# Kernel optimization log

Hardware: AMD Instinct MI355X
Metric: run time of the kernel (lower is better)

## Reference

```python
import jax, jax.numpy as jnp
import numpy as np


def setup_inputs() -> dict:
    key = jax.random.key(0)
    k0, k1, k2, k3 = jax.random.split(key, 4)
    N, D, DEG, B = 20000, 128, 32, 1024
    features = jax.random.normal(k0, (N, D), jnp.float32)
    neighbors = jax.random.randint(k1, (N, DEG), 0, N, dtype=jnp.int32)
    train_index = jax.random.randint(k2, (B,), 0, N, dtype=jnp.int32)
    W = jax.random.normal(k3, (1, 2 * D), jnp.float32) * (1.0 / np.sqrt(2 * D))
    b = jnp.zeros((1,), jnp.float32)
    return {"features": features, "W": W, "b": b, "neighbors": neighbors,
            "train_index": train_index, "walk_times": 8, "batch_size": B}


def reference(features, W, b, neighbors, train_index, walk_times, batch_size):
    N, D = features.shape
    B = train_index.shape[0]
    rows = jnp.arange(B)[:, None]                       # [B,1]
    self_oh = jax.nn.one_hot(train_index, N, dtype=jnp.float32)  # [B,N]

    # Dense adjacency rows of the start nodes (== adj_sparse[batch] densified)
    nb0 = neighbors[train_index]                        # [B,deg]
    adj0 = jnp.zeros((B, N), jnp.float32).at[rows, nb0].set(1.0)

    chosen = self_oh                                    # visited mask (start node marked)
    candi_mask = (adj0 - chosen) > 0.0                  # non-self candidates

    # Per-edge learned score: relu(Linear(concat(f_x, f_y))) == relu(fx@Wx + fy@Wy + b)
    Wx, Wy = W[0, :D], W[0, D:]
    sx = features[train_index] @ Wx                     # [B]
    sy = features[nb0] @ Wy                             # [B,deg]
    s = jax.nn.relu(sx[:, None] + sy + b[0])            # [B,deg]
    scored = jnp.zeros((B, N), jnp.float32).at[rows, nb0].set(s)
    candi = jnp.where(candi_mask, scored, 0.0)
    # rows with no (or all-zero-scored) candidates fall back to a self-loop of weight 1
    candi = jnp.where((candi.sum(axis=1) == 0.0)[:, None], self_oh, candi)

    keys = jax.random.split(jax.random.key(42), walk_times)

    def step(carry, k):
        candi, chosen = carry
        # degenerate rows: resample the start node (safe fallback for empty support)
        p = jnp.where((candi.sum(axis=1) == 0.0)[:, None], self_oh, candi)
        # multinomial(p, 1) via Gumbel-max (categorical with probs proportional to p)
        logp = jnp.where(p > 0.0, jnp.log(jnp.where(p > 0.0, p, 1.0)), -jnp.inf)
        g = jax.random.gumbel(k, (p.shape[0], p.shape[1]), jnp.float32)
        new = jnp.argmax(logp + g, axis=1)              # [B]
        chosen = jnp.maximum(chosen, jax.nn.one_hot(new, p.shape[1], dtype=jnp.float32))
        adj_new = jnp.zeros_like(candi).at[rows, neighbors[new]].set(1.0)
        candi = ((candi - chosen + adj_new) > 0.0).astype(jnp.float32)
        return (candi, chosen), new

    (_, _), steps = jax.lax.scan(step, (candi, chosen), keys)  # steps: [T,B]
    walks = jnp.concatenate(
        [train_index[:, None].astype(jnp.int32), steps.T.astype(jnp.int32)], axis=1)
    return walks
```

## Files before the change

kernel.cpp:

```cpp
#include <hip/hip_runtime.h>
#include <cstdint>

namespace {

constexpr int N    = 20000;
constexpr int D    = 128;
constexpr int DEG  = 32;
constexpr int BB   = 1024;
constexpr int T    = 8;
constexpr int NC   = (N + 15) / 16;
constexpr int MAXC = 384;

__device__ __forceinline__ uint32_t rotl32(uint32_t x, int n) {
  return (x << n) | (x >> (32 - n));
}

__device__ __forceinline__ void threefry2x32(uint32_t k0, uint32_t k1,
                                             uint32_t x0, uint32_t x1,
                                             uint32_t& o0, uint32_t& o1) {
  const uint32_t ks2 = k0 ^ k1 ^ 0x1BD11BDAu;
  x0 += k0; x1 += k1;
#define TF_ROUND(r) { x0 += x1; x1 = rotl32(x1, (r)); x1 ^= x0; }
  TF_ROUND(13) TF_ROUND(15) TF_ROUND(26) TF_ROUND(6)
  x0 += k1;  x1 += ks2 + 1u;
  TF_ROUND(17) TF_ROUND(29) TF_ROUND(16) TF_ROUND(24)
  x0 += ks2; x1 += k0 + 2u;
  TF_ROUND(13) TF_ROUND(15) TF_ROUND(26) TF_ROUND(6)
  x0 += k0;  x1 += k1 + 3u;
  TF_ROUND(17) TF_ROUND(29) TF_ROUND(16) TF_ROUND(24)
  x0 += k1;  x1 += ks2 + 4u;
  TF_ROUND(13) TF_ROUND(15) TF_ROUND(26) TF_ROUND(6)
  x0 += ks2; x1 += k0 + 5u;
#undef TF_ROUND
  o0 = x0; o1 = x1;
}

__device__ __forceinline__ uint32_t rbits(uint32_t k0, uint32_t k1, uint32_t j) {
  uint32_t o0, o1;
  threefry2x32(k0, k1, 0u, j, o0, o1);
  return o0 ^ o1;
}

__device__ __forceinline__ float gumbel_f32(uint32_t bits) {
  const uint32_t mant = bits >> 9;
  const float u = (mant == 0u) ? 1.17549435e-38f
                               : (__uint_as_float(0x3F800000u | mant) - 1.0f);
  const float inner = -(float)log((double)u);
  return -(float)log((double)inner);
}

__device__ __forceinline__ uint32_t f2ord(float f) {
  const uint32_t b = __float_as_uint(f);
  return (b & 0x80000000u) ? ~b : (b | 0x80000000u);
}

template <int CTRL>
__device__ __forceinline__ uint32_t dppmov(uint32_t v) {
  return (uint32_t)__builtin_amdgcn_update_dpp((int)v, (int)v, CTRL, 0xF, 0xF, false);
}

__device__ __forceinline__ void wave_max64(uint32_t& hi, uint32_t& lo) {
#define RL(CTRL) { const uint32_t oh = dppmov<CTRL>(hi), ol = dppmov<CTRL>(lo); \
    if (oh > hi || (oh == hi && ol > lo)) { hi = oh; lo = ol; } }
  RL(0x111) RL(0x112) RL(0x114) RL(0x118) RL(0x142) RL(0x143)
#undef RL
  hi = (uint32_t)__builtin_amdgcn_readlane((int)hi, 63);
  lo = (uint32_t)__builtin_amdgcn_readlane((int)lo, 63);
}

__device__ __forceinline__ uint32_t cwd(int n)  { return (uint32_t)n >> 4; }
__device__ __forceinline__ uint32_t cbit(int n) { return 1u << (((uint32_t)n & 15u) << 1); }

__global__ __launch_bounds__(64)
void walk_kernel(const float* __restrict__ features,
                 const float* __restrict__ W,
                 const float* __restrict__ bptr,
                 const int*   __restrict__ neighbors,
                 const int*   __restrict__ train_index,
                 int* __restrict__ out)
{
  __shared__ uint32_t comb[NC];
  __shared__ int      lst[MAXC];
  __shared__ float    val0[DEG];

  const int lane = threadIdx.x;
  const int r    = blockIdx.x;
  const int self = train_index[r];
  const uint32_t rN = (uint32_t)(r * N);
  const uint64_t lower = (1ULL << lane) - 1ULL;

  int nbj = -1;
  if (lane < DEG) nbj = neighbors[(size_t)self * DEG + lane];

  {
    uint64_t* c8 = reinterpret_cast<uint64_t*>(comb);
    for (int i = lane; i < NC / 2; i += 64) c8[i] = 0ull;
  }

  uint32_t sk0, sk1;
  threefry2x32(0u, 42u, 0u, (uint32_t)lane, sk0, sk1);

  const float bval = bptr[0];
  const float* frow = features + (size_t)self * D;
  float acc = frow[lane] * W[lane] + frow[lane + 64] * W[lane + 64];
  for (int m = 1; m < 64; m <<= 1) acc += __shfl_xor(acc, m);
  const float sx = acc;

  float sval = 0.0f;
  if (lane < DEG) {
    const float* g  = features + (size_t)nbj * D;
    const float* wy = W + D;
    float a = 0.0f;
    for (int d = 0; d < D; d += 4) {
      const float4 f = *reinterpret_cast<const float4*>(g + d);
      const float4 w = *reinterpret_cast<const float4*>(wy + d);
      a += f.x * w.x; a += f.y * w.y; a += f.z * w.z; a += f.w * w.w;
    }
    sval = fmaxf((sx + a) + bval, 0.0f);
  }

  bool add0 = false;
  if (lane < DEG && nbj != self && sval > 0.0f) {
    const uint32_t old = atomicOr(&comb[cwd(nbj)], cbit(nbj));
    add0 = !(old & cbit(nbj));
  }
  const uint64_t m0 = __ballot(add0);
  if (add0) {
    const int p = (int)__popcll(m0 & lower);
    lst[p] = nbj; val0[p] = sval;
  }
  int cnt = (int)__popcll(m0);
  if (lane == 0) {
    atomicOr(&comb[cwd(self)], cbit(self) << 1);
    if (cnt == 0) {
      lst[0] = self; val0[0] = 1.0f;
      atomicOr(&comb[cwd(self)], cbit(self));
    }
  }
  if (cnt == 0) cnt = 1;

  int zom0 = 0, zom1 = 0, zom2 = 0, zom3 = 0, zmask = 0;
  uint32_t hiP = 0u, loP = 0u;

  for (int k = 0; k < T; ++k) {
    uint32_t hi, lo;
    if (k == 0) {
      const uint32_t kk0 = (uint32_t)__builtin_amdgcn_readlane((int)sk0, 0);
      const uint32_t kk1 = (uint32_t)__builtin_amdgcn_readlane((int)sk1, 0);
      hi = 0u; lo = 0u;
      if (lane < cnt) {
        const int c = lst[lane];
        const float v = (float)log((double)val0[lane])
                      + gumbel_f32(rbits(kk0, kk1, rN + (uint32_t)c));
        hi = f2ord(v); lo = ((0x7FFFFFu - (uint32_t)c) << 9) | (uint32_t)lane;
      }
    } else {
      hi = hiP; lo = loP;
    }
    wave_max64(hi, lo);
    const bool haveList = (cnt > 0);
    const int nn  = haveList ? (int)(0x7FFFFFu - (lo >> 9)) : self;
    const int pos = (int)(lo & 0x1FFu);

    if (lane == 0) out[r * (T + 1) + k + 1] = nn;
    if (k == T - 1) break;

    int nb = -1;
    if (lane < DEG) nb = neighbors[(size_t)nn * DEG + lane];

    if (lane == 0) atomicOr(&comb[cwd(nn)], cbit(nn) << 1);

    float v0f = 1.0f;
    if (k == 0 && haveList) v0f = val0[pos];

    if (haveList) {
      const int last = lst[cnt - 1];
      if (pos != cnt - 1 && lane == 0) lst[pos] = last;
      --cnt;
    }

    const uint32_t nk0 = (uint32_t)__builtin_amdgcn_readlane((int)sk0, k + 1);
    const uint32_t nk1 = (uint32_t)__builtin_amdgcn_readlane((int)sk1, k + 1);

    hiP = 0u; loP = 0u;
    for (int i = lane; i < cnt; i += 64) {
      const int c = lst[i];
      const uint32_t h = rbits(nk0, nk1, rN + (uint32_t)c) >> 9;
      const uint32_t l = ((0x7FFFFFu - (uint32_t)c) << 9) | (uint32_t)i;
      if (h > hiP || (h == hiP && l > loP)) { hiP = h; loP = l; }
    }

    const bool adNN = __any(nb == nn);
    const bool wasZ = ((zmask & 1) && zom0 == nn) || ((zmask & 2) && zom1 == nn) ||
                      ((zmask & 4) && zom2 == nn) || ((zmask & 8) && zom3 == nn);
    const bool stay = haveList &&
        ((k == 0) ? (((v0f - 1.0f) + (adNN ? 1.0f : 0.0f)) > 0.0f) : adNN);

    if (stay) {
      if (lane == 0) lst[cnt] = nn;
      const int posN = cnt; ++cnt;
      if (!wasZ) {
        if      (!(zmask & 1)) { zom0 = nn; zmask |= 1; }
        else if (!(zmask & 2)) { zom1 = nn; zmask |= 2; }
        else if (!(zmask & 4)) { zom2 = nn; zmask |= 4; }
        else                   { zom3 = nn; zmask |= 8; }
      }
      const uint32_t h = rbits(nk0, nk1, rN + (uint32_t)nn) >> 9;
      const uint32_t l = ((0x7FFFFFu - (uint32_t)nn) << 9) | (uint32_t)posN;
      if (h > hiP || (h == hiP && l > loP)) { hiP = h; loP = l; }
    } else if (wasZ) {
      if ((zmask & 1) && zom0 == nn) zmask &= ~1;
      else if ((zmask & 2) && zom1 == nn) zmask &= ~2;
      else if ((zmask & 4) && zom2 == nn) zmask &= ~4;
      else if ((zmask & 8) && zom3 == nn) zmask &= ~8;
    }

    bool zdrop = false;
    if (zmask) {
#define ZTEST(BIT, Z) \
      if ((zmask & BIT) && Z != nn) { \
        if (!__any(nb == Z)) { \
          int pz = -1; \
          for (int i = lane; i < cnt; i += 64) if (lst[i] == Z) pz = i; \
          const uint64_t fz = __ballot(pz >= 0); \
          const int sz = (int)(__ffsll((unsigned long long)fz) - 1); \
          pz = __shfl(pz, sz); \
          const int lastz = lst[cnt - 1]; \
          if (pz != cnt - 1 && lane == 0) lst[pz] = lastz; \
          --cnt; zmask &= ~BIT; zdrop = true; \
        } \
      }
      ZTEST(1, zom0) ZTEST(2, zom1) ZTEST(4, zom2) ZTEST(8, zom3)
#undef ZTEST
    }
    if (zdrop) {
      hiP = 0u; loP = 0u;
      for (int i = lane; i < cnt; i += 64) {
        const int c = lst[i];
        const uint32_t h = rbits(nk0, nk1, rN + (uint32_t)c) >> 9;
        const uint32_t l = ((0x7FFFFFu - (uint32_t)c) << 9) | (uint32_t)i;
        if (h > hiP || (h == hiP && l > loP)) { hiP = h; loP = l; }
      }
    }

    uint32_t hN = 0u;
    if (lane < DEG) hN = rbits(nk0, nk1, rN + (uint32_t)nb) >> 9;
    bool added = false;
    if (lane < DEG) {
      const uint32_t old = atomicOr(&comb[cwd(nb)], cbit(nb));
      added = !(old & (cbit(nb) | (cbit(nb) << 1)));
    }
    const uint64_t ma = __ballot(added);
    const int mypos = cnt + (int)__popcll(ma & lower);
    if (added) {
      lst[mypos] = nb;
      const uint32_t l = ((0x7FFFFFu - (uint32_t)nb) << 9) | (uint32_t)mypos;
      if (hN > hiP || (hN == hiP && l > loP)) { hiP = hN; loP = l; }
    }
    cnt += (int)__popcll(ma);
  }
  if (lane == 0) out[r * (T + 1)] = self;
}

}

extern "C" void kernel_launch(void* const* d_in, const int* in_sizes, int n_in,
                              void* d_out, int out_size, void* d_ws, size_t ws_size,
                              hipStream_t stream) {
  const float* features  = (const float*)d_in[0];
  const float* W         = (const float*)d_in[1];
  const float* b         = (const float*)d_in[2];
  const int*   neighbors = (const int*)d_in[3];
  const int*   tindex    = (const int*)d_in[4];
  int* out = (int*)d_out;

  hipLaunchKernelGGL(walk_kernel, dim3(BB), dim3(64), 0, stream,
                     features, W, b, neighbors, tindex, out);
}
```

Baseline: 24.12 us.

## Pack two walk rows per wavefront using 32-lane halves

Each 64-lane wavefront now handles two batch rows, one per 32-lane half, with separate shared visited bitmaps and candidate lists, and the grid is halved to BB/2 blocks. Before, lanes 32-63 sat idle during the neighbor-degree work. Reductions become half-wave DPP reductions that read lanes 31 and 63, and ballots are shifted per half. The cost is divergence when the two halves take different branches (zombie tests, list scans), which serializes their work, plus a doubled shared-memory footprint per block.

```diff
diff --git a/kernel.cpp b/kernel.cpp
--- a/kernel.cpp
+++ b/kernel.cpp
@@ -59,13 +59,16 @@
   return (uint32_t)__builtin_amdgcn_update_dpp((int)v, (int)v, CTRL, 0xF, 0xF, false);
 }
 
-__device__ __forceinline__ void wave_max64(uint32_t& hi, uint32_t& lo) {
+__device__ __forceinline__ void wave_max64_half(uint32_t& hi, uint32_t& lo, int half) {
 #define RL(CTRL) { const uint32_t oh = dppmov<CTRL>(hi), ol = dppmov<CTRL>(lo); \
     if (oh > hi || (oh == hi && ol > lo)) { hi = oh; lo = ol; } }
-  RL(0x111) RL(0x112) RL(0x114) RL(0x118) RL(0x142) RL(0x143)
+  RL(0x111) RL(0x112) RL(0x114) RL(0x118) RL(0x142)
 #undef RL
-  hi = (uint32_t)__builtin_amdgcn_readlane((int)hi, 63);
-  lo = (uint32_t)__builtin_amdgcn_readlane((int)lo, 63);
+  const uint32_t hA = (uint32_t)__builtin_amdgcn_readlane((int)hi, 31);
+  const uint32_t lA = (uint32_t)__builtin_amdgcn_readlane((int)lo, 31);
+  const uint32_t hB = (uint32_t)__builtin_amdgcn_readlane((int)hi, 63);
+  const uint32_t lB = (uint32_t)__builtin_amdgcn_readlane((int)lo, 63);
+  hi = half ? hB : hA; lo = half ? lB : lA;
 }
 
 __device__ __forceinline__ uint32_t cwd(int n)  { return (uint32_t)n >> 4; }
@@ -79,62 +82,68 @@
                  const int*   __restrict__ train_index,
                  int* __restrict__ out)
 {
-  __shared__ uint32_t comb[NC];
-  __shared__ int      lst[MAXC];
-  __shared__ float    val0[DEG];
+  __shared__ __align__(8) uint32_t comb[2][NC];
+  __shared__ int      lst[2][MAXC];
+  __shared__ float    val0[2][DEG];
 
   const int lane = threadIdx.x;
-  const int r    = blockIdx.x;
+  const int half = lane >> 5;
+  const int hl   = lane & 31;
+  const int bid  = blockIdx.x;
+  const int r    = bid + half * (BB / 2);
   const int self = train_index[r];
   const uint32_t rN = (uint32_t)(r * N);
-  const uint64_t lower = (1ULL << lane) - 1ULL;
-
-  int nbj = -1;
-  if (lane < DEG) nbj = neighbors[(size_t)self * DEG + lane];
+  const uint32_t lowerH = (1u << hl) - 1u;
+
+  const int nbj = neighbors[(size_t)self * DEG + hl];
 
   {
-    uint64_t* c8 = reinterpret_cast<uint64_t*>(comb);
-    for (int i = lane; i < NC / 2; i += 64) c8[i] = 0ull;
+    uint64_t* c8 = reinterpret_cast<uint64_t*>(&comb[0][0]);
+    for (int i = lane; i < NC; i += 64) c8[i] = 0ull;
   }
 
   uint32_t sk0, sk1;
   threefry2x32(0u, 42u, 0u, (uint32_t)lane, sk0, sk1);
 
   const float bval = bptr[0];
-  const float* frow = features + (size_t)self * D;
-  float acc = frow[lane] * W[lane] + frow[lane + 64] * W[lane + 64];
-  for (int m = 1; m < 64; m <<= 1) acc += __shfl_xor(acc, m);
-  const float sx = acc;
-
-  float sval = 0.0f;
-  if (lane < DEG) {
+  const int selfA = __shfl(self, 0);
+  const int selfB = __shfl(self, 32);
+  const float* frowA = features + (size_t)selfA * D;
+  float accA = frowA[lane] * W[lane] + frowA[lane + 64] * W[lane + 64];
+  for (int m = 1; m < 64; m <<= 1) accA += __shfl_xor(accA, m);
+  const float* frowB = features + (size_t)selfB * D;
+  float accB = frowB[lane] * W[lane] + frowB[lane + 64] * W[lane + 64];
+  for (int m = 1; m < 64; m <<= 1) accB += __shfl_xor(accB, m);
+  const float sx = half ? accB : accA;
+
+  float a = 0.0f;
+  {
     const float* g  = features + (size_t)nbj * D;
     const float* wy = W + D;
-    float a = 0.0f;
     for (int d = 0; d < D; d += 4) {
       const float4 f = *reinterpret_cast<const float4*>(g + d);
       const float4 w = *reinterpret_cast<const float4*>(wy + d);
       a += f.x * w.x; a += f.y * w.y; a += f.z * w.z; a += f.w * w.w;
     }
-    sval = fmaxf((sx + a) + bval, 0.0f);
-  }
-
-  bool add0 = false;
-  if (lane < DEG && nbj != self && sval > 0.0f) {
-    const uint32_t old = atomicOr(&comb[cwd(nbj)], cbit(nbj));
+  }
+  const float sval = fmaxf((sx + a) + bval, 0.0f);
+
+  bool add0 = (nbj != self && sval > 0.0f);
+  if (add0) {
+    const uint32_t old = atomicOr(&comb[half][cwd(nbj)], cbit(nbj));
     add0 = !(old & cbit(nbj));
   }
-  const uint64_t m0 = __ballot(add0);
+  const uint32_t m0 = (uint32_t)(__ballot(add0) >> (half << 5));
   if (add0) {
-    const int p = (int)__popcll(m0 & lower);
-    lst[p] = nbj; val0[p] = sval;
-  }
-  int cnt = (int)__popcll(m0);
-  if (lane == 0) {
-    atomicOr(&comb[cwd(self)], cbit(self) << 1);
+    const int p = (int)__popc(m0 & lowerH);
+    lst[half][p] = nbj; val0[half][p] = sval;
+  }
+  int cnt = (int)__popc(m0);
+  if (hl == 0) {
+    atomicOr(&comb[half][cwd(self)], cbit(self) << 1);
     if (cnt == 0) {
-      lst[0] = self; val0[0] = 1.0f;
-      atomicOr(&comb[cwd(self)], cbit(self));
+      lst[half][0] = self; val0[half][0] = 1.0f;
+      atomicOr(&comb[half][cwd(self)], cbit(self));
     }
   }
   if (cnt == 0) cnt = 1;
@@ -148,34 +157,34 @@
       const uint32_t kk0 = (uint32_t)__builtin_amdgcn_readlane((int)sk0, 0);
       const uint32_t kk1 = (uint32_t)__builtin_amdgcn_readlane((int)sk1, 0);
       hi = 0u; lo = 0u;
-      if (lane < cnt) {
-        const int c = lst[lane];
-        const float v = (float)log((double)val0[lane])
+      if (hl < cnt) {
+        const int c = lst[half][hl];
+        const float v = (float)log((double)val0[half][hl])
                       + gumbel_f32(rbits(kk0, kk1, rN + (uint32_t)c));
-        hi = f2ord(v); lo = ((0x7FFFFFu - (uint32_t)c) << 9) | (uint32_t)lane;
+        hi = f2ord(v); lo = ((0x7FFFFFu - (uint32_t)c) << 9) | (uint32_t)hl;
       }
     } else {
       hi = hiP; lo = loP;
     }
-    wave_max64(hi, lo);
+    wave_max64_half(hi, lo, half);
     const bool haveList = (cnt > 0);
     const int nn  = haveList ? (int)(0x7FFFFFu - (lo >> 9)) : self;
     const int pos = (int)(lo & 0x1FFu);
 
-    if (lane == 0) out[r * (T + 1) + k + 1] = nn;
+    if (hl == 0) out[r * (T + 1) + k + 1] = nn;
     if (k == T - 1) break;
 
-    int nb = -1;
-    if (lane < DEG) nb = neighbors[(size_t)nn * DEG + lane];
-
-    if (lane == 0) atomicOr(&comb[cwd(nn)], cbit(nn) << 1);
+    const int nb = neighbors[(size_t)nn * DEG + hl];
+
+    if (hl == 0) atomicOr(&comb[half][cwd(nn)], cbit(nn) << 1);
 
     float v0f = 1.0f;
-    if (k == 0 && haveList) v0f = val0[pos];
+    if (k == 0 && haveList) v0f = val0[half][pos];
+    int last = 0;
+    if (haveList) last = lst[half][cnt - 1];
 
     if (haveList) {
-      const int last = lst[cnt - 1];
-      if (pos != cnt - 1 && lane == 0) lst[pos] = last;
+      if (pos != cnt - 1 && hl == 0) lst[half][pos] = last;
       --cnt;
     }
 
@@ -183,21 +192,21 @@
     const uint32_t nk1 = (uint32_t)__builtin_amdgcn_readlane((int)sk1, k + 1);
 
     hiP = 0u; loP = 0u;
-    for (int i = lane; i < cnt; i += 64) {
-      const int c = lst[i];
+    for (int i = hl; i < cnt; i += 32) {
+      const int c = lst[half][i];
       const uint32_t h = rbits(nk0, nk1, rN + (uint32_t)c) >> 9;
       const uint32_t l = ((0x7FFFFFu - (uint32_t)c) << 9) | (uint32_t)i;
       if (h > hiP || (h == hiP && l > loP)) { hiP = h; loP = l; }
     }
 
-    const bool adNN = __any(nb == nn);
+    const bool adNN = ((uint32_t)(__ballot(nb == nn) >> (half << 5))) != 0u;
     const bool wasZ = ((zmask & 1) && zom0 == nn) || ((zmask & 2) && zom1 == nn) ||
                       ((zmask & 4) && zom2 == nn) || ((zmask & 8) && zom3 == nn);
     const bool stay = haveList &&
         ((k == 0) ? (((v0f - 1.0f) + (adNN ? 1.0f : 0.0f)) > 0.0f) : adNN);
 
     if (stay) {
-      if (lane == 0) lst[cnt] = nn;
+      if (hl == 0) lst[half][cnt] = nn;
       const int posN = cnt; ++cnt;
       if (!wasZ) {
         if      (!(zmask & 1)) { zom0 = nn; zmask |= 1; }
@@ -219,14 +228,14 @@
     if (zmask) {
 #define ZTEST(BIT, Z) \
       if ((zmask & BIT) && Z != nn) { \
-        if (!__any(nb == Z)) { \
+        if (((uint32_t)(__ballot(nb == Z) >> (half << 5))) == 0u) { \
           int pz = -1; \
-          for (int i = lane; i < cnt; i += 64) if (lst[i] == Z) pz = i; \
-          const uint64_t fz = __ballot(pz >= 0); \
-          const int sz = (int)(__ffsll((unsigned long long)fz) - 1); \
+          for (int i = hl; i < cnt; i += 32) if (lst[half][i] == Z) pz = i; \
+          const uint32_t fz = (uint32_t)(__ballot(pz >= 0) >> (half << 5)); \
+          const int sz = (half << 5) + (__ffs(fz) - 1); \
           pz = __shfl(pz, sz); \
-          const int lastz = lst[cnt - 1]; \
-          if (pz != cnt - 1 && lane == 0) lst[pz] = lastz; \
+          const int lastz = lst[half][cnt - 1]; \
+          if (pz != cnt - 1 && hl == 0) lst[half][pz] = lastz; \
           --cnt; zmask &= ~BIT; zdrop = true; \
         } \
       }
@@ -235,31 +244,27 @@
     }
     if (zdrop) {
       hiP = 0u; loP = 0u;
-      for (int i = lane; i < cnt; i += 64) {
-        const int c = lst[i];
+      for (int i = hl; i < cnt; i += 32) {
+        const int c = lst[half][i];
         const uint32_t h = rbits(nk0, nk1, rN + (uint32_t)c) >> 9;
         const uint32_t l = ((0x7FFFFFu - (uint32_t)c) << 9) | (uint32_t)i;
         if (h > hiP || (h == hiP && l > loP)) { hiP = h; loP = l; }
       }
     }
 
-    uint32_t hN = 0u;
-    if (lane < DEG) hN = rbits(nk0, nk1, rN + (uint32_t)nb) >> 9;
-    bool added = false;
-    if (lane < DEG) {
-      const uint32_t old = atomicOr(&comb[cwd(nb)], cbit(nb));
-      added = !(old & (cbit(nb) | (cbit(nb) << 1)));
-    }
-    const uint64_t ma = __ballot(added);
-    const int mypos = cnt + (int)__popcll(ma & lower);
+    const uint32_t hN = rbits(nk0, nk1, rN + (uint32_t)nb) >> 9;
+    const uint32_t old = atomicOr(&comb[half][cwd(nb)], cbit(nb));
+    const bool added = !(old & (cbit(nb) | (cbit(nb) << 1)));
+    const uint32_t ma = (uint32_t)(__ballot(added) >> (half << 5));
+    const int mypos = cnt + (int)__popc(ma & lowerH);
     if (added) {
-      lst[mypos] = nb;
+      lst[half][mypos] = nb;
       const uint32_t l = ((0x7FFFFFu - (uint32_t)nb) << 9) | (uint32_t)mypos;
       if (hN > hiP || (hN == hiP && l > loP)) { hiP = hN; loP = l; }
     }
-    cnt += (int)__popcll(ma);
-  }
-  if (lane == 0) out[r * (T + 1)] = self;
+    cnt += (int)__popc(ma);
+  }
+  if (hl == 0) out[r * (T + 1)] = self;
 }
 
 }
@@ -274,6 +279,6 @@
   const int*   tindex    = (const int*)d_in[4];
   int* out = (int*)d_out;
 
-  hipLaunchKernelGGL(walk_kernel, dim3(BB), dim3(64), 0, stream,
+  hipLaunchKernelGGL(walk_kernel, dim3(BB / 2), dim3(64), 0, stream,
                      features, W, b, neighbors, tindex, out);
 }
```

Result: slower. 26.32 us (+9.1%).

## Keep candidate list in per-lane registers instead of shared memory

Applied to the files above, without the earlier changes.

Moves the candidate node list from a shared-memory array into five per-lane register slots (c0..c4), and uses readlane for lookups and lane-predicated writes for swap-removal and insertion. Newly added neighbours are still written to a shared staging buffer and then copied into the register slots. The goal is to drop LDS reads from the per-step scoring loops and the removal searches. In exchange it adds branchy slot selection and more register use, and it caps capacity at 320 entries where the shared array held 384.

```diff
diff --git a/kernel.cpp b/kernel.cpp
--- a/kernel.cpp
+++ b/kernel.cpp
@@ -3,13 +3,14 @@
 
 namespace {
 
-constexpr int N    = 20000;
-constexpr int D    = 128;
-constexpr int DEG  = 32;
-constexpr int BB   = 1024;
-constexpr int T    = 8;
-constexpr int NC   = (N + 15) / 16;
-constexpr int MAXC = 384;
+constexpr int N     = 20000;
+constexpr int D     = 128;
+constexpr int DEG   = 32;
+constexpr int BB    = 1024;
+constexpr int T     = 8;
+constexpr int NC    = (N + 15) / 16;
+constexpr int MAXC  = 320;
+constexpr int SLOTS = 5;
 
 __device__ __forceinline__ uint32_t rotl32(uint32_t x, int n) {
   return (x << n) | (x >> (32 - n));
@@ -71,6 +72,8 @@
 __device__ __forceinline__ uint32_t cwd(int n)  { return (uint32_t)n >> 4; }
 __device__ __forceinline__ uint32_t cbit(int n) { return 1u << (((uint32_t)n & 15u) << 1); }
 
+#define GETC(S) ((S)==0?c0:(S)==1?c1:(S)==2?c2:(S)==3?c3:c4)
+
 __global__ __launch_bounds__(64)
 void walk_kernel(const float* __restrict__ features,
                  const float* __restrict__ W,
@@ -79,8 +82,8 @@
                  const int*   __restrict__ train_index,
                  int* __restrict__ out)
 {
-  __shared__ uint32_t comb[NC];
-  __shared__ int      lst[MAXC];
+  __shared__ __align__(8) uint32_t comb[NC];
+  __shared__ int      stage[MAXC];
   __shared__ float    val0[DEG];
 
   const int lane = threadIdx.x;
@@ -88,6 +91,8 @@
   const int self = train_index[r];
   const uint32_t rN = (uint32_t)(r * N);
   const uint64_t lower = (1ULL << lane) - 1ULL;
+
+  int c0 = 0, c1 = 0, c2 = 0, c3 = 0, c4 = 0;
 
   int nbj = -1;
   if (lane < DEG) nbj = neighbors[(size_t)self * DEG + lane];
@@ -127,17 +132,22 @@
   const uint64_t m0 = __ballot(add0);
   if (add0) {
     const int p = (int)__popcll(m0 & lower);
-    lst[p] = nbj; val0[p] = sval;
+    stage[p] = nbj; val0[p] = sval;
   }
   int cnt = (int)__popcll(m0);
   if (lane == 0) {
     atomicOr(&comb[cwd(self)], cbit(self) << 1);
     if (cnt == 0) {
-      lst[0] = self; val0[0] = 1.0f;
+      val0[0] = 1.0f;
       atomicOr(&comb[cwd(self)], cbit(self));
     }
   }
-  if (cnt == 0) cnt = 1;
+  if (cnt == 0) {
+    if (lane == 0) c0 = self;
+    cnt = 1;
+  } else if (lane < cnt) {
+    c0 = stage[lane];
+  }
 
   int zom0 = 0, zom1 = 0, zom2 = 0, zom3 = 0, zmask = 0;
   uint32_t hiP = 0u, loP = 0u;
@@ -149,7 +159,7 @@
       const uint32_t kk1 = (uint32_t)__builtin_amdgcn_readlane((int)sk1, 0);
       hi = 0u; lo = 0u;
       if (lane < cnt) {
-        const int c = lst[lane];
+        const int c = c0;
         const float v = (float)log((double)val0[lane])
                       + gumbel_f32(rbits(kk0, kk1, rN + (uint32_t)c));
         hi = f2ord(v); lo = ((0x7FFFFFu - (uint32_t)c) << 9) | (uint32_t)lane;
@@ -174,8 +184,23 @@
     if (k == 0 && haveList) v0f = val0[pos];
 
     if (haveList) {
-      const int last = lst[cnt - 1];
-      if (pos != cnt - 1 && lane == 0) lst[pos] = last;
+      const int li = cnt - 1;
+      int last;
+      { const int ls = li >> 6, ll = li & 63;
+        if      (ls == 0) last = __builtin_amdgcn_readlane(c0, ll);
+        else if (ls == 1) last = __builtin_amdgcn_readlane(c1, ll);
+        else if (ls == 2) last = __builtin_amdgcn_readlane(c2, ll);
+        else if (ls == 3) last = __builtin_amdgcn_readlane(c3, ll);
+        else              last = __builtin_amdgcn_readlane(c4, ll);
+      }
+      if (pos != li) {
+        const int ps = pos >> 6, pl = pos & 63;
+        if      (ps == 0) { if (lane == pl) c0 = last; }
+        else if (ps == 1) { if (lane == pl) c1 = last; }
+        else if (ps == 2) { if (lane == pl) c2 = last; }
+        else if (ps == 3) { if (lane == pl) c3 = last; }
+        else              { if (lane == pl) c4 = last; }
+      }
       --cnt;
     }
 
@@ -183,11 +208,15 @@
     const uint32_t nk1 = (uint32_t)__builtin_amdgcn_readlane((int)sk1, k + 1);
 
     hiP = 0u; loP = 0u;
-    for (int i = lane; i < cnt; i += 64) {
-      const int c = lst[i];
-      const uint32_t h = rbits(nk0, nk1, rN + (uint32_t)c) >> 9;
-      const uint32_t l = ((0x7FFFFFu - (uint32_t)c) << 9) | (uint32_t)i;
-      if (h > hiP || (h == hiP && l > loP)) { hiP = h; loP = l; }
+#pragma unroll
+    for (int s = 0; s < SLOTS; ++s) {
+      const int idx = s * 64 + lane;
+      if (idx < cnt) {
+        const int c = GETC(s);
+        const uint32_t h = rbits(nk0, nk1, rN + (uint32_t)c) >> 9;
+        const uint32_t l = ((0x7FFFFFu - (uint32_t)c) << 9) | (uint32_t)idx;
+        if (h > hiP || (h == hiP && l > loP)) { hiP = h; loP = l; }
+      }
     }
 
     const bool adNN = __any(nb == nn);
@@ -197,8 +226,15 @@
         ((k == 0) ? (((v0f - 1.0f) + (adNN ? 1.0f : 0.0f)) > 0.0f) : adNN);
 
     if (stay) {
-      if (lane == 0) lst[cnt] = nn;
-      const int posN = cnt; ++cnt;
+      const int posN = cnt;
+      { const int ps = posN >> 6, pl = posN & 63;
+        if      (ps == 0) { if (lane == pl) c0 = nn; }
+        else if (ps == 1) { if (lane == pl) c1 = nn; }
+        else if (ps == 2) { if (lane == pl) c2 = nn; }
+        else if (ps == 3) { if (lane == pl) c3 = nn; }
+        else              { if (lane == pl) c4 = nn; }
+      }
+      ++cnt;
       if (!wasZ) {
         if      (!(zmask & 1)) { zom0 = nn; zmask |= 1; }
         else if (!(zmask & 2)) { zom1 = nn; zmask |= 2; }
@@ -221,12 +257,31 @@
       if ((zmask & BIT) && Z != nn) { \
         if (!__any(nb == Z)) { \
           int pz = -1; \
-          for (int i = lane; i < cnt; i += 64) if (lst[i] == Z) pz = i; \
+          if (0 * 64 + lane < cnt && c0 == Z) pz = 0 * 64 + lane; \
+          if (1 * 64 + lane < cnt && c1 == Z) pz = 1 * 64 + lane; \
+          if (2 * 64 + lane < cnt && c2 == Z) pz = 2 * 64 + lane; \
+          if (3 * 64 + lane < cnt && c3 == Z) pz = 3 * 64 + lane; \
+          if (4 * 64 + lane < cnt && c4 == Z) pz = 4 * 64 + lane; \
           const uint64_t fz = __ballot(pz >= 0); \
           const int sz = (int)(__ffsll((unsigned long long)fz) - 1); \
           pz = __shfl(pz, sz); \
-          const int lastz = lst[cnt - 1]; \
-          if (pz != cnt - 1 && lane == 0) lst[pz] = lastz; \
+          const int li = cnt - 1; \
+          int lastz; \
+          { const int ls = li >> 6, ll = li & 63; \
+            if      (ls == 0) lastz = __builtin_amdgcn_readlane(c0, ll); \
+            else if (ls == 1) lastz = __builtin_amdgcn_readlane(c1, ll); \
+            else if (ls == 2) lastz = __builtin_amdgcn_readlane(c2, ll); \
+            else if (ls == 3) lastz = __builtin_amdgcn_readlane(c3, ll); \
+            else              lastz = __builtin_amdgcn_readlane(c4, ll); \
+          } \
+          if (pz != li) { \
+            const int ps = pz >> 6, pl = pz & 63; \
+            if      (ps == 0) { if (lane == pl) c0 = lastz; } \
+            else if (ps == 1) { if (lane == pl) c1 = lastz; } \
+            else if (ps == 2) { if (lane == pl) c2 = lastz; } \
+            else if (ps == 3) { if (lane == pl) c3 = lastz; } \
+            else              { if (lane == pl) c4 = lastz; } \
+          } \
           --cnt; zmask &= ~BIT; zdrop = true; \
         } \
       }
@@ -235,11 +290,15 @@
     }
     if (zdrop) {
       hiP = 0u; loP = 0u;
-      for (int i = lane; i < cnt; i += 64) {
-        const int c = lst[i];
-        const uint32_t h = rbits(nk0, nk1, rN + (uint32_t)c) >> 9;
-        const uint32_t l = ((0x7FFFFFu - (uint32_t)c) << 9) | (uint32_t)i;
-        if (h > hiP || (h == hiP && l > loP)) { hiP = h; loP = l; }
+#pragma unroll
+      for (int s = 0; s < SLOTS; ++s) {
+        const int idx = s * 64 + lane;
+        if (idx < cnt) {
+          const int c = GETC(s);
+          const uint32_t h = rbits(nk0, nk1, rN + (uint32_t)c) >> 9;
+          const uint32_t l = ((0x7FFFFFu - (uint32_t)c) << 9) | (uint32_t)idx;
+          if (h > hiP || (h == hiP && l > loP)) { hiP = h; loP = l; }
+        }
       }
     }
 
@@ -253,11 +312,24 @@
     const uint64_t ma = __ballot(added);
     const int mypos = cnt + (int)__popcll(ma & lower);
     if (added) {
-      lst[mypos] = nb;
+      stage[mypos] = nb;
       const uint32_t l = ((0x7FFFFFu - (uint32_t)nb) << 9) | (uint32_t)mypos;
       if (hN > hiP || (hN == hiP && l > loP)) { hiP = hN; loP = l; }
     }
-    cnt += (int)__popcll(ma);
+    const int cntNew = cnt + (int)__popcll(ma);
+#pragma unroll
+    for (int s = 0; s < SLOTS; ++s) {
+      const int idx = s * 64 + lane;
+      if (idx >= cnt && idx < cntNew) {
+        const int v = stage[idx];
+        if      (s == 0) c0 = v;
+        else if (s == 1) c1 = v;
+        else if (s == 2) c2 = v;
+        else if (s == 3) c3 = v;
+        else             c4 = v;
+      }
+    }
+    cnt = cntNew;
   }
   if (lane == 0) out[r * (T + 1)] = self;
 }
```

Measured after the change: 25.30 us. 1.05x slower.
